# Kernel tuning notes

Hardware: AMD Instinct MI355X
Metric: run time of the kernel (lower is better)

Reference implementation:

```python
import jax, jax.numpy as jnp
import numpy as np

NA, NB = 50000, 10000        # node counts for types 'a' and 'b'
D_IN, D_OUT = 32, 64         # input feature dim, GRU hidden / GAT out dim
EA2A, EA2B, EB2A = 800000, 400000, 400000


def setup_inputs() -> dict:
    key = jax.random.key(0)
    ks = jax.random.split(key, 17)
    f32 = jnp.float32
    inp = {
        'x_a': jax.random.normal(ks[0], (NA, D_IN), f32),
        'x_b': jax.random.normal(ks[1], (NB, D_IN), f32),
        'h_a': jax.random.normal(ks[2], (NA, D_OUT), f32),
        'h_b': jax.random.normal(ks[3], (NB, D_OUT), f32),
        # stacked params: axis0 = gate (z,r,n); axis1 = node type (a,b) or edge type (a2a,a2b,b2a)
        'Wx': jax.random.normal(ks[4], (3, 2, D_IN, D_OUT), f32) * 0.05,
        'bx': jax.random.normal(ks[5], (3, 2, D_OUT), f32) * 0.05,
        'gat_ws': jax.random.normal(ks[6], (3, 3, D_OUT, D_OUT), f32) * 0.05,
        'gat_wd': jax.random.normal(ks[7], (3, 3, D_OUT, D_OUT), f32) * 0.05,
        'gat_as': jax.random.normal(ks[8], (3, 3, D_OUT), f32) * 0.05,
        'gat_ad': jax.random.normal(ks[9], (3, 3, D_OUT), f32) * 0.05,
        'gat_b': jax.random.normal(ks[10], (3, 3, D_OUT), f32) * 0.05,
        'ea2a_src': jax.random.randint(ks[11], (EA2A,), 0, NA, jnp.int32),
        'ea2a_dst': jax.random.randint(ks[12], (EA2A,), 0, NA, jnp.int32),
        'ea2b_src': jax.random.randint(ks[13], (EA2B,), 0, NA, jnp.int32),
        'ea2b_dst': jax.random.randint(ks[14], (EA2B,), 0, NB, jnp.int32),
        'eb2a_src': jax.random.randint(ks[15], (EB2A,), 0, NB, jnp.int32),
        'eb2a_dst': jax.random.randint(ks[16], (EB2A,), 0, NA, jnp.int32),
    }
    return inp


def _gat(hs, hd, src, dst, w_s, w_d, a_s, a_d, b, n_dst):
    """Single-head GATConv (PyG semantics, add_self_loops=False)."""
    xs = hs @ w_s                                   # [Ns, D] transformed sources
    xd = hd @ w_d                                   # [Nd, D] transformed destinations
    al_s = xs @ a_s                                 # [Ns]
    al_d = xd @ a_d                                 # [Nd]
    e = jax.nn.leaky_relu(al_s[src] + al_d[dst], 0.2)   # [E] raw attention logits
    m = jax.ops.segment_max(e, dst, num_segments=n_dst)
    m = jnp.where(jnp.isfinite(m), m, 0.0)          # empty segments -> 0 (unused)
    ex = jnp.exp(e - m[dst])
    denom = jax.ops.segment_sum(ex, dst, num_segments=n_dst)
    alpha = ex / (denom[dst] + 1e-16)               # segment softmax over in-edges
    out = jax.ops.segment_sum(alpha[:, None] * xs[src], dst, num_segments=n_dst)
    return out + b


def _hetero_conv(ha, hb, ws, wd, a_s, a_d, b, edges):
    """HeteroConv with sum aggregation across edge types per destination type."""
    (sa2a, da2a), (sa2b, da2b), (sb2a, db2a) = edges
    out_a = (_gat(ha, ha, sa2a, da2a, ws[0], wd[0], a_s[0], a_d[0], b[0], NA)
             + _gat(hb, ha, sb2a, db2a, ws[2], wd[2], a_s[2], a_d[2], b[2], NA))
    out_b = _gat(ha, hb, sa2b, da2b, ws[1], wd[1], a_s[1], a_d[1], b[1], NB)
    return out_a, out_b


def reference(x_a, x_b, h_a, h_b, Wx, bx, gat_ws, gat_wd, gat_as, gat_ad, gat_b,
              ea2a_src, ea2a_dst, ea2b_src, ea2b_dst, eb2a_src, eb2a_dst):
    edges = ((ea2a_src, ea2a_dst), (ea2b_src, ea2b_dst), (eb2a_src, eb2a_dst))

    def gate(g, ha_in, hb_in, act):
        ca, cb = _hetero_conv(ha_in, hb_in, gat_ws[g], gat_wd[g],
                              gat_as[g], gat_ad[g], gat_b[g], edges)
        ga = act(x_a @ Wx[g, 0] + ca + bx[g, 0])
        gb = act(x_b @ Wx[g, 1] + cb + bx[g, 1])
        return ga, gb

    z_a, z_b = gate(0, h_a, h_b, jax.nn.sigmoid)          # update gate
    r_a, r_b = gate(1, h_a, h_b, jax.nn.sigmoid)          # reset gate
    n_a, n_b = gate(2, r_a * h_a, r_b * h_b, jnp.tanh)    # candidate state
    new_a = (1.0 - z_a) * n_a + z_a * h_a
    new_b = (1.0 - z_b) * n_b + z_b * h_b
    return jnp.concatenate([new_a, new_b], axis=0)        # [NA+NB, D_OUT]
```

## Files before the change

kernel.cpp:

```cpp
#include <hip/hip_runtime.h>
#include <hip/hip_bf16.h>
#include <cstddef>
#include <cstdint>

#define NA 50000
#define NB 10000
#define D_IN 32
#define D_OUT 64
#define EA2A 800000
#define EA2B 400000
#define EB2A 400000
#define NCAT (NA + NB + NA)
#define ETOT (EA2A + EA2B + EB2A)
#define NCHUNK 8
#define CHUNK (NCAT / NCHUNK)
#define NSLICE 64
#define ESLICE (ETOT / NSLICE)

typedef unsigned int u32;
typedef unsigned short u16;
typedef __attribute__((ext_vector_type(8))) short short8_t;
typedef __attribute__((ext_vector_type(4))) float f32x4;
typedef __attribute__((ext_vector_type(2))) float f32x2;

__device__ __forceinline__ u32 bf16r(float x) {
    u32 u = __float_as_uint(x);
    u += 0x7fffu + ((u >> 16) & 1u);
    return u >> 16;
}
__device__ __forceinline__ float ubf(u32 bits) { return __uint_as_float(bits); }
__device__ __forceinline__ float sigm(float x) { return 1.f / (1.f + __expf(-x)); }
__device__ __forceinline__ u32 cvtpk(float lo, float hi) {
    u32 r;
    asm("v_cvt_pk_bf16_f32 %0, %1, %2" : "=v"(r) : "v"(lo), "v"(hi));
    return r;
}
__device__ __forceinline__ void pkfma(f32x2& acc, f32x2 x, f32x2 p) {
    asm("v_pk_fma_f32 %0, %1, %2, %0" : "+v"(acc) : "v"(x), "v"(p));
}

template <int CTRL, int RM>
__device__ __forceinline__ float dppf(float v) {
    return __int_as_float(__builtin_amdgcn_update_dpp(0, __float_as_int(v), CTRL, RM, 0xf, true));
}
__device__ __forceinline__ float wsum64(float v) {
    v += dppf<0x111, 0xf>(v);
    v += dppf<0x112, 0xf>(v);
    v += dppf<0x114, 0xf>(v);
    v += dppf<0x118, 0xf>(v);
    v += dppf<0x142, 0xa>(v);
    v += dppf<0x143, 0xc>(v);
    return __int_as_float(__builtin_amdgcn_readlane(__float_as_int(v), 63));
}

struct MmArgs {
    const float* H; int ntiles;
    const float* W0; const float* W1;
    void* XS;
    const float* SW[8]; const float* SA[8]; float* SOUT[8];
    int sstride; int nsc;
};

template <int NMAT>
__global__ void __launch_bounds__(256) gemm_mfma(MmArgs a)
{
    __shared__ float wvec[8][64];
    __shared__ short8_t bfr[NMAT * 8 + 2][64];
    int t = threadIdx.x;
    for (int idx = t; idx < a.nsc * 64; idx += 256) {
        int c = idx >> 6, k = idx & 63;
        const float* w = a.SW[c] + k * 64;
        const float* av = a.SA[c];
        float s = 0.f;
#pragma unroll 16
        for (int e = 0; e < 64; ++e) s = fmaf(w[e], av[e], s);
        wvec[c][k] = s;
    }
    __syncthreads();
    for (int idx = t; idx < NMAT * 8 * 64; idx += 256) {
        int fid = idx >> 6, l = idx & 63;
        int m = fid >> 3, r3 = fid & 7, tn = r3 >> 1, q = r3 & 1;
        const float* W = (NMAT == 2 && m == 1) ? a.W1 : a.W0;
        int kbase = 32 * q + ((l >> 4) << 3);
        int d = 16 * tn + (l & 15);
        short8_t v;
#pragma unroll
        for (int e = 0; e < 8; ++e) v[e] = (short)bf16r(W[(size_t)(kbase + e) * 64 + d]);
        bfr[fid][l] = v;
    }
    for (int idx = t; idx < 128; idx += 256) {
        int q = idx >> 6, l = idx & 63;
        int c = l & 15;
        int kbase = 32 * q + ((l >> 4) << 3);
        short8_t v;
#pragma unroll
        for (int e = 0; e < 8; ++e) v[e] = (c < a.nsc) ? (short)bf16r(wvec[c][kbase + e]) : (short)0;
        bfr[NMAT * 8 + q][l] = v;
    }
    __syncthreads();
    int lane = t & 63, wid = t >> 6;
    short8_t bw[NMAT][4][2], bs0, bs1;
#pragma unroll
    for (int m = 0; m < NMAT; ++m)
#pragma unroll
        for (int tn = 0; tn < 4; ++tn)
#pragma unroll
            for (int q = 0; q < 2; ++q) bw[m][tn][q] = bfr[m * 8 + tn * 2 + q][lane];
    bs0 = bfr[NMAT * 8][lane];
    bs1 = bfr[NMAT * 8 + 1][lane];

    int rl = lane & 15, kg = lane >> 4;
    f32x4 zero = {0.f, 0.f, 0.f, 0.f};
    for (int tile = blockIdx.x * 4 + wid; tile < a.ntiles; tile += gridDim.x * 4) {
        const float4* hp = (const float4*)(a.H + (size_t)(tile * 16 + rl) * 64) + kg * 2;
        float4 a0 = hp[0], a1 = hp[1];
        float4 b0 = hp[8], b1 = hp[9];
        union { short8_t s; u32 w[4]; } A0, A1;
        A0.w[0] = cvtpk(a0.x, a0.y); A0.w[1] = cvtpk(a0.z, a0.w);
        A0.w[2] = cvtpk(a1.x, a1.y); A0.w[3] = cvtpk(a1.z, a1.w);
        A1.w[0] = cvtpk(b0.x, b0.y); A1.w[1] = cvtpk(b0.z, b0.w);
        A1.w[2] = cvtpk(b1.x, b1.y); A1.w[3] = cvtpk(b1.z, b1.w);

        f32x4 acc[NMAT][4];
#pragma unroll
        for (int m = 0; m < NMAT; ++m)
#pragma unroll
            for (int tn = 0; tn < 4; ++tn) {
                f32x4 c0 = __builtin_amdgcn_mfma_f32_16x16x32_bf16(A0.s, bw[m][tn][0], zero, 0, 0, 0);
                acc[m][tn] = __builtin_amdgcn_mfma_f32_16x16x32_bf16(A1.s, bw[m][tn][1], c0, 0, 0, 0);
            }
        f32x4 accs = __builtin_amdgcn_mfma_f32_16x16x32_bf16(A0.s, bs0, zero, 0, 0, 0);
        accs = __builtin_amdgcn_mfma_f32_16x16x32_bf16(A1.s, bs1, accs, 0, 0, 0);

        int rbase = tile * 16 + kg * 4;
        if (NMAT == 2) {
            u32* xo = (u32*)a.XS;
#pragma unroll
            for (int tn = 0; tn < 4; ++tn) {
                int d = tn * 16 + rl;
#pragma unroll
                for (int j = 0; j < 4; ++j)
                    xo[(size_t)(rbase + j) * 64 + d] = cvtpk(acc[0][tn][j], acc[1][tn][j]);
            }
        } else {
            u16* xo = (u16*)a.XS;
#pragma unroll
            for (int tn = 0; tn < 4; ++tn) {
                int d = tn * 16 + rl;
#pragma unroll
                for (int j = 0; j < 4; ++j)
                    xo[(size_t)(rbase + j) * 64 + d] = (u16)bf16r(acc[0][tn][j]);
            }
        }
        if (rl < a.nsc) {
            float* so = a.SOUT[rl];
#pragma unroll
            for (int j = 0; j < 4; ++j) so[(size_t)(rbase + j) * a.sstride] = accs[j];
        }
    }
}

__global__ void __launch_bounds__(256) gemm_x_k(
    const float* __restrict__ xA, const float* __restrict__ xB,
    const float* __restrict__ Wx, const float* __restrict__ bx, const float* __restrict__ gb,
    u32* __restrict__ dzrA, u32* __restrict__ dzrB,
    u16* __restrict__ dnA, u16* __restrict__ dnB)
{
    __shared__ float Wsh[3 * 2048];
    __shared__ float cb[3 * 64];
    int t = threadIdx.x;
    int blk = blockIdx.x;
    bool isA = blk < (NA / 8);
    int ty = isA ? 0 : 1;
#pragma unroll
    for (int g = 0; g < 3; ++g) {
        const float4* s = (const float4*)(Wx + (size_t)(g * 2 + ty) * 2048);
        float4* d = (float4*)&Wsh[g * 2048];
        for (int i = t; i < 512; i += 256) d[i] = s[i];
    }
    if (t < 192) {
        int g = t >> 6, d = t & 63;
        float c = bx[(g * 2 + ty) * 64 + d];
        if (isA) c += gb[(g * 3 + 0) * 64 + d] + gb[(g * 3 + 2) * 64 + d];
        else     c += gb[(g * 3 + 1) * 64 + d];
        cb[t] = c;
    }
    __syncthreads();
    int lane = t & 63, wid = t >> 6;
    const float* X = isA ? xA : xB;
    int N = isA ? NA : NB;
    int rbase = (isA ? blk : blk - NA / 8) * 8 + wid * 2;
    float cz = cb[lane], cr = cb[64 + lane], cn = cb[128 + lane];
#pragma unroll
    for (int rr = 0; rr < 2; ++rr) {
        int r = rbase + rr;
        if (r >= N) break;
        float xv = (lane < 32) ? X[(size_t)r * 32 + lane] : 0.f;
        float az = cz, ar = cr, an = cn;
#pragma unroll
        for (int k = 0; k < 32; ++k) {
            float xk = __shfl(xv, k, 64);
            az = fmaf(xk, Wsh[k * 64 + lane], az);
            ar = fmaf(xk, Wsh[2048 + k * 64 + lane], ar);
            an = fmaf(xk, Wsh[4096 + k * 64 + lane], an);
        }
        u32 zr = bf16r(az) | (bf16r(ar) << 16);
        u16 nn = (u16)bf16r(an);
        if (isA) { dzrA[(size_t)r * 64 + lane] = zr; dnA[(size_t)r * 64 + lane] = nn; }
        else     { dzrB[(size_t)r * 64 + lane] = zr; dnB[(size_t)r * 64 + lane] = nn; }
    }
}

__global__ void __launch_bounds__(512) hist_k(
    const int* __restrict__ d0, const int* __restrict__ d1, const int* __restrict__ d2,
    u16* __restrict__ partial)
{
    __shared__ int hcnt[CHUNK];
    int k = blockIdx.x & (NCHUNK - 1);
    int s = blockIdx.x / NCHUNK;
    int lo = k * CHUNK;
    for (int i = threadIdx.x; i < CHUNK; i += 512) hcnt[i] = 0;
    __syncthreads();
    int e0 = s * ESLICE, e1 = e0 + ESLICE;
    for (int e = e0 + threadIdx.x; e < e1; e += 512) {
        int g;
        if (e < EA2A) g = d0[e];
        else if (e < EA2A + EA2B) g = NA + d1[e - EA2A];
        else g = NA + NB + d2[e - EA2A - EA2B];
        u32 rel = (u32)(g - lo);
        if (rel < CHUNK) atomicAdd(&hcnt[rel], 1);
    }
    __syncthreads();
    u16* po = partial + (size_t)s * NCAT + lo;
    for (int i = threadIdx.x; i < CHUNK; i += 512) po[i] = (u16)hcnt[i];
}

__global__ void scan_partial(const u16* __restrict__ partial, int* __restrict__ bsum, int N)
{
    __shared__ int sd[256];
    int t = threadIdx.x;
    int i = blockIdx.x * 256 + t;
    int v = 0;
    if (i < N) {
#pragma unroll 16
        for (int s = 0; s < NSLICE; ++s) v += partial[(size_t)s * NCAT + i];
    }
    sd[t] = v;
    __syncthreads();
    for (int off = 128; off; off >>= 1) {
        if (t < off) sd[t] += sd[t + off];
        __syncthreads();
    }
    if (t == 0) bsum[blockIdx.x] = sd[0];
}

__global__ void __launch_bounds__(512) scan_tops(int* bsum, int nb)
{
    __shared__ int sd[512];
    int t = threadIdx.x;
    int v = (t < nb) ? bsum[t] : 0;
    sd[t] = v;
    __syncthreads();
    for (int off = 1; off < 512; off <<= 1) {
        int add = (t >= off) ? sd[t - off] : 0;
        __syncthreads();
        sd[t] += add;
        __syncthreads();
    }
    if (t < nb) bsum[t] = sd[t] - v;
}

__global__ void scan_final(const u16* __restrict__ partial, const int* __restrict__ bsum,
                           int* __restrict__ rowptr, int* __restrict__ cnt,
                           u32* __restrict__ soff, int N)
{
    __shared__ int sd[256];
    int t = threadIdx.x;
    int i = blockIdx.x * 256 + t;
    int v = 0;
    if (i < N) {
#pragma unroll 16
        for (int s = 0; s < NSLICE; ++s) v += partial[(size_t)s * NCAT + i];
    }
    sd[t] = v;
    __syncthreads();
    for (int off = 1; off < 256; off <<= 1) {
        int add = (t >= off) ? sd[t - off] : 0;
        __syncthreads();
        sd[t] += add;
        __syncthreads();
    }
    if (i < N) {
        int rpi = bsum[blockIdx.x] + sd[t] - v;
        rowptr[i] = rpi;
        cnt[i] = v;
        int run = rpi;
#pragma unroll 16
        for (int s = 0; s < NSLICE; ++s) {
            soff[(size_t)s * NCAT + i] = (u32)run;
            run += partial[(size_t)s * NCAT + i];
        }
    }
}

__global__ void __launch_bounds__(512) fill_k(
    const int* __restrict__ s0, const int* __restrict__ d0,
    const int* __restrict__ s1, const int* __restrict__ d1,
    const int* __restrict__ s2, const int* __restrict__ d2,
    const u32* __restrict__ soff, u16* __restrict__ csr)
{
    __shared__ int fpos[CHUNK];
    int k = blockIdx.x & (NCHUNK - 1);
    int s = blockIdx.x / NCHUNK;
    int lo = k * CHUNK;
    const u32* po = soff + (size_t)s * NCAT + lo;
    for (int i = threadIdx.x; i < CHUNK; i += 512) fpos[i] = (int)po[i];
    __syncthreads();
    int e0 = s * ESLICE, e1 = e0 + ESLICE;
    for (int e = e0 + threadIdx.x; e < e1; e += 512) {
        int g, sidx;
        const int* sp;
        if (e < EA2A) { g = d0[e]; sp = s0; sidx = e; }
        else if (e < EA2A + EA2B) { sidx = e - EA2A; g = NA + d1[sidx]; sp = s1; }
        else { sidx = e - EA2A - EA2B; g = NA + NB + d2[sidx]; sp = s2; }
        u32 rel = (u32)(g - lo);
        if (rel < CHUNK) {
            int src = sp[sidx];
            int p = atomicAdd(&fpos[rel], 1);
            csr[p] = (u16)src;
        }
    }
}

__device__ __forceinline__ void zr_pk(f32x2 azr[4], uint4 v, f32x2 p) {
    f32x2 x;
    x[0] = ubf(v.x << 16); x[1] = ubf(v.x & 0xffff0000u); pkfma(azr[0], x, p);
    x[0] = ubf(v.y << 16); x[1] = ubf(v.y & 0xffff0000u); pkfma(azr[1], x, p);
    x[0] = ubf(v.z << 16); x[1] = ubf(v.z & 0xffff0000u); pkfma(azr[2], x, p);
    x[0] = ubf(v.w << 16); x[1] = ubf(v.w & 0xffff0000u); pkfma(azr[3], x, p);
}

__device__ __forceinline__ void gat_zr_et(
    int gnode, int inode, int lane, int sub, int grp,
    const int* __restrict__ rp, const int* __restrict__ cnt, const u16* __restrict__ csr,
    const float2* __restrict__ als, const float2* __restrict__ ald,
    const uint4* __restrict__ xs,
    float oz[4], float orr[4])
{
    int deg = cnt[gnode];
    if (deg <= 0) return;
    int beg = rp[gnode];
    float2 ad = ald[inode];
    f32x2 azr[4];
#pragma unroll
    for (int q = 0; q < 4; ++q) { azr[q][0] = 0.f; azr[q][1] = 0.f; }
    float szl = 0.f, srl = 0.f;
    for (int base = 0; base < deg; base += 64) {
        int j = base + lane;
        int sj = 0; float pz = 0.f, pr = 0.f;
        if (j < deg) {
            sj = csr[beg + j];
            float2 al = als[sj];
            float tz = al.x + ad.x;
            float tr = al.y + ad.y;
            pz = __expf(fmaxf(tz, 0.2f * tz));
            pr = __expf(fmaxf(tr, 0.2f * tr));
        }
        szl += pz; srl += pr;
        u32 pk = (u32)sj | (bf16r(pz) << 16);
        int c = deg - base; if (c > 64) c = 64;
        int b = 0;
        for (; b + 16 <= c; b += 16) {
            u32 k0 = (u32)__shfl((int)pk, b + grp, 64);
            u32 k1 = (u32)__shfl((int)pk, b + 4 + grp, 64);
            u32 k2 = (u32)__shfl((int)pk, b + 8 + grp, 64);
            u32 k3 = (u32)__shfl((int)pk, b + 12 + grp, 64);
            float q0 = __shfl(pr, b + grp, 64);
            float q1 = __shfl(pr, b + 4 + grp, 64);
            float q2 = __shfl(pr, b + 8 + grp, 64);
            float q3 = __shfl(pr, b + 12 + grp, 64);
            uint4 v0 = xs[(size_t)(k0 & 0xffffu) * 16 + sub];
            uint4 v1 = xs[(size_t)(k1 & 0xffffu) * 16 + sub];
            uint4 v2 = xs[(size_t)(k2 & 0xffffu) * 16 + sub];
            uint4 v3 = xs[(size_t)(k3 & 0xffffu) * 16 + sub];
            f32x2 p;
            p[0] = ubf(k0 & 0xffff0000u); p[1] = q0; zr_pk(azr, v0, p);
            p[0] = ubf(k1 & 0xffff0000u); p[1] = q1; zr_pk(azr, v1, p);
            p[0] = ubf(k2 & 0xffff0000u); p[1] = q2; zr_pk(azr, v2, p);
            p[0] = ubf(k3 & 0xffff0000u); p[1] = q3; zr_pk(azr, v3, p);
        }
        for (; b < c; b += 4) {
            u32 k0 = (u32)__shfl((int)pk, b + grp, 64);
            float q0 = __shfl(pr, b + grp, 64);
            uint4 v0 = xs[(size_t)(k0 & 0xffffu) * 16 + sub];
            f32x2 p;
            p[0] = ubf(k0 & 0xffff0000u); p[1] = q0;
            zr_pk(azr, v0, p);
        }
    }
    float sz = wsum64(szl), sr = wsum64(srl);
    float rz = 1.f / (sz + 1e-16f), rr = 1.f / (sr + 1e-16f);
#pragma unroll
    for (int q = 0; q < 4; ++q) {
        oz[q] = fmaf(azr[q][0], rz, oz[q]);
        orr[q] = fmaf(azr[q][1], rr, orr[q]);
    }
}

__device__ __forceinline__ void n_pk(f32x2 ac[2], uint2 v, f32x2 p) {
    f32x2 x;
    x[0] = ubf(v.x << 16); x[1] = ubf(v.x & 0xffff0000u); pkfma(ac[0], x, p);
    x[0] = ubf(v.y << 16); x[1] = ubf(v.y & 0xffff0000u); pkfma(ac[1], x, p);
}

__device__ __forceinline__ void gat_n_et(
    int gnode, int inode, int lane, int sub, int grp,
    const int* __restrict__ rp, const int* __restrict__ cnt, const u16* __restrict__ csr,
    const float* __restrict__ als, const float* __restrict__ ald,
    const uint2* __restrict__ xs,
    float oa[4])
{
    int deg = cnt[gnode];
    if (deg <= 0) return;
    int beg = rp[gnode];
    float ad = ald[inode];
    f32x2 ac[2];
    ac[0][0] = 0.f; ac[0][1] = 0.f; ac[1][0] = 0.f; ac[1][1] = 0.f;
    float ssl = 0.f;
    for (int base = 0; base < deg; base += 64) {
        int j = base + lane;
        int sj = 0; float pv = 0.f;
        if (j < deg) {
            sj = csr[beg + j];
            float tv = als[sj] + ad;
            pv = __expf(fmaxf(tv, 0.2f * tv));
        }
        ssl += pv;
        u32 pk = (u32)sj | (bf16r(pv) << 16);
        int c = deg - base; if (c > 64) c = 64;
        int b = 0;
        for (; b + 16 <= c; b += 16) {
            u32 k0 = (u32)__shfl((int)pk, b + grp, 64);
            u32 k1 = (u32)__shfl((int)pk, b + 4 + grp, 64);
            u32 k2 = (u32)__shfl((int)pk, b + 8 + grp, 64);
            u32 k3 = (u32)__shfl((int)pk, b + 12 + grp, 64);
            uint2 v0 = xs[(size_t)(k0 & 0xffffu) * 16 + sub];
            uint2 v1 = xs[(size_t)(k1 & 0xffffu) * 16 + sub];
            uint2 v2 = xs[(size_t)(k2 & 0xffffu) * 16 + sub];
            uint2 v3 = xs[(size_t)(k3 & 0xffffu) * 16 + sub];
            f32x2 p;
            p[0] = ubf(k0 & 0xffff0000u); p[1] = p[0]; n_pk(ac, v0, p);
            p[0] = ubf(k1 & 0xffff0000u); p[1] = p[0]; n_pk(ac, v1, p);
            p[0] = ubf(k2 & 0xffff0000u); p[1] = p[0]; n_pk(ac, v2, p);
            p[0] = ubf(k3 & 0xffff0000u); p[1] = p[0]; n_pk(ac, v3, p);
        }
        for (; b < c; b += 4) {
            u32 k0 = (u32)__shfl((int)pk, b + grp, 64);
            uint2 v0 = xs[(size_t)(k0 & 0xffffu) * 16 + sub];
            f32x2 p;
            p[0] = ubf(k0 & 0xffff0000u); p[1] = p[0];
            n_pk(ac, v0, p);
        }
    }
    float ss = wsum64(ssl);
    float rs = 1.f / (ss + 1e-16f);
    oa[0] = fmaf(ac[0][0], rs, oa[0]);
    oa[1] = fmaf(ac[0][1], rs, oa[1]);
    oa[2] = fmaf(ac[1][0], rs, oa[2]);
    oa[3] = fmaf(ac[1][1], rs, oa[3]);
}

struct ZrArgs {
    const int *rp, *cnt;
    const u16 *csr;
    const float2 *als0, *ald0, *als1, *ald1, *als2, *ald2;
    const uint4 *xs0, *xs1, *xs2;
    const u32 *dzrA, *dzrB;
    const float *hA, *hB;
    float *zA, *rhA, *zB, *rhB;
};

__global__ void __launch_bounds__(256) aggregate_zr_k(ZrArgs P)
{
    int t = threadIdx.x, lane = t & 63, wid = t >> 6;
    int sub = lane & 15, grp = lane >> 4;
    float oz[4] = {0.f, 0.f, 0.f, 0.f}, orr[4] = {0.f, 0.f, 0.f, 0.f};
    int blk = blockIdx.x;
    const u32* dzr; const float* Hp; float *Zp, *RHp;
    if (blk < NA / 4) {
        int i = blk * 4 + wid;
        gat_zr_et(i, i, lane, sub, grp, P.rp, P.cnt, P.csr, P.als0, P.ald0, P.xs0, oz, orr);
        gat_zr_et(NA + NB + i, i, lane, sub, grp, P.rp, P.cnt, P.csr, P.als2, P.ald2, P.xs2, oz, orr);
        dzr = P.dzrA + (size_t)i * 64; Hp = P.hA + (size_t)i * 64;
        Zp = P.zA + (size_t)i * 64; RHp = P.rhA + (size_t)i * 64;
    } else {
        int i = (blk - NA / 4) * 4 + wid;
        gat_zr_et(NA + i, i, lane, sub, grp, P.rp, P.cnt, P.csr, P.als1, P.ald1, P.xs1, oz, orr);
        dzr = P.dzrB + (size_t)i * 64; Hp = P.hB + (size_t)i * 64;
        Zp = P.zB + (size_t)i * 64; RHp = P.rhB + (size_t)i * 64;
    }
#pragma unroll
    for (int q = 0; q < 4; ++q) {
        oz[q] += __shfl_xor(oz[q], 16, 64); oz[q] += __shfl_xor(oz[q], 32, 64);
        orr[q] += __shfl_xor(orr[q], 16, 64); orr[q] += __shfl_xor(orr[q], 32, 64);
    }
    if (grp == 0) {
        uint4 d = *(const uint4*)(dzr + sub * 4);
        float4 h = *(const float4*)(Hp + sub * 4);
        float z0 = sigm(oz[0] + ubf(d.x << 16)), r0 = sigm(orr[0] + ubf(d.x & 0xffff0000u)) * h.x;
        float z1 = sigm(oz[1] + ubf(d.y << 16)), r1 = sigm(orr[1] + ubf(d.y & 0xffff0000u)) * h.y;
        float z2 = sigm(oz[2] + ubf(d.z << 16)), r2 = sigm(orr[2] + ubf(d.z & 0xffff0000u)) * h.z;
        float z3 = sigm(oz[3] + ubf(d.w << 16)), r3 = sigm(orr[3] + ubf(d.w & 0xffff0000u)) * h.w;
        *(float4*)(Zp + sub * 4) = make_float4(z0, z1, z2, z3);
        *(float4*)(RHp + sub * 4) = make_float4(r0, r1, r2, r3);
    }
}

struct NArgs {
    const int *rp, *cnt;
    const u16 *csr;
    const float *als0, *ald0, *als1, *ald1, *als2, *ald2;
    const uint2 *xs0, *xs1, *xs2;
    const u16 *dnA, *dnB;
    const float *hA, *hB, *zA, *zB;
    float *outA, *outB;
};

__global__ void __launch_bounds__(256) aggregate_n_k(NArgs P)
{
    int t = threadIdx.x, lane = t & 63, wid = t >> 6;
    int sub = lane & 15, grp = lane >> 4;
    float oa[4] = {0.f, 0.f, 0.f, 0.f};
    int blk = blockIdx.x;
    const u16* dn; const float *Hp, *Zp; float* Op;
    if (blk < NA / 4) {
        int i = blk * 4 + wid;
        gat_n_et(i, i, lane, sub, grp, P.rp, P.cnt, P.csr, P.als0, P.ald0, P.xs0, oa);
        gat_n_et(NA + NB + i, i, lane, sub, grp, P.rp, P.cnt, P.csr, P.als2, P.ald2, P.xs2, oa);
        dn = P.dnA + (size_t)i * 64; Hp = P.hA + (size_t)i * 64;
        Zp = P.zA + (size_t)i * 64; Op = P.outA + (size_t)i * 64;
    } else {
        int i = (blk - NA / 4) * 4 + wid;
        gat_n_et(NA + i, i, lane, sub, grp, P.rp, P.cnt, P.csr, P.als1, P.ald1, P.xs1, oa);
        dn = P.dnB + (size_t)i * 64; Hp = P.hB + (size_t)i * 64;
        Zp = P.zB + (size_t)i * 64; Op = P.outB + (size_t)i * 64;
    }
#pragma unroll
    for (int q = 0; q < 4; ++q) {
        oa[q] += __shfl_xor(oa[q], 16, 64); oa[q] += __shfl_xor(oa[q], 32, 64);
    }
    if (grp == 0) {
        uint2 d = *(const uint2*)(dn + sub * 4);
        float4 h = *(const float4*)(Hp + sub * 4);
        float4 zv = *(const float4*)(Zp + sub * 4);
        float pre[4];
        pre[0] = oa[0] + ubf(d.x << 16);
        pre[1] = oa[1] + ubf(d.x & 0xffff0000u);
        pre[2] = oa[2] + ubf(d.y << 16);
        pre[3] = oa[3] + ubf(d.y & 0xffff0000u);
        float o[4];
        float hh[4] = {h.x, h.y, h.z, h.w};
        float zz[4] = {zv.x, zv.y, zv.z, zv.w};
#pragma unroll
        for (int q = 0; q < 4; ++q) {
            float x2 = fminf(fmaxf(pre[q] * 2.f, -30.f), 30.f);
            float ex = __expf(x2);
            float nv = (ex - 1.f) / (ex + 1.f);
            o[q] = (1.f - zz[q]) * nv + zz[q] * hh[q];
        }
        *(float4*)(Op + sub * 4) = make_float4(o[0], o[1], o[2], o[3]);
    }
}

extern "C" void kernel_launch(void* const* d_in, const int* in_sizes, int n_in,
                              void* d_out, int out_size, void* d_ws, size_t ws_size,
                              hipStream_t stream)
{
    (void)in_sizes; (void)n_in; (void)out_size; (void)ws_size;
    const float* x_a = (const float*)d_in[0];
    const float* x_b = (const float*)d_in[1];
    const float* h_a = (const float*)d_in[2];
    const float* h_b = (const float*)d_in[3];
    const float* Wx  = (const float*)d_in[4];
    const float* bx  = (const float*)d_in[5];
    const float* gws = (const float*)d_in[6];
    const float* gwd = (const float*)d_in[7];
    const float* gas = (const float*)d_in[8];
    const float* gad = (const float*)d_in[9];
    const float* gb  = (const float*)d_in[10];
    const int* ea2a_s = (const int*)d_in[11];
    const int* ea2a_d = (const int*)d_in[12];
    const int* ea2b_s = (const int*)d_in[13];
    const int* ea2b_d = (const int*)d_in[14];
    const int* eb2a_s = (const int*)d_in[15];
    const int* eb2a_d = (const int*)d_in[16];
    float* out = (float*)d_out;

    char* w = (char*)d_ws;
    auto alloc = [&](size_t bytes) -> char* {
        char* p = w;
        w += (bytes + 255) & ~(size_t)255;
        return p;
    };
    char* xsblk = alloc((size_t)(NA + NA + NB) * 64 * 4);
    u32* xs_zr0 = (u32*)xsblk;
    u32* xs_zr1 = (u32*)(xsblk + (size_t)NA * 64 * 4);
    u32* xs_zr2 = (u32*)(xsblk + (size_t)(NA + NA) * 64 * 4);
    u16* xs_n0 = (u16*)xsblk;
    u16* xs_n1 = (u16*)(xsblk + (size_t)NA * 64 * 2);
    u16* xs_n2 = (u16*)(xsblk + (size_t)(NA + NA) * 64 * 2);
    char* alblk = alloc((size_t)(4 * NA + 2 * NB) * 2 * 4);
    float* als_zr0 = (float*)alblk;
    float* als_zr1 = als_zr0 + (size_t)NA * 2;
    float* als_zr2 = als_zr1 + (size_t)NA * 2;
    float* ald_zr0 = als_zr2 + (size_t)NB * 2;
    float* ald_zr1 = ald_zr0 + (size_t)NA * 2;
    float* ald_zr2 = ald_zr1 + (size_t)NB * 2;
    float* als_n0 = (float*)alblk;
    float* als_n1 = als_n0 + NA;
    float* als_n2 = als_n1 + NA;
    float* ald_n0 = als_n2 + NB;
    float* ald_n1 = ald_n0 + NA;
    float* ald_n2 = ald_n1 + NB;
    float* zbuf  = (float*)alloc((size_t)(NA + NB) * 64 * 4);
    float* rhbuf = (float*)alloc((size_t)(NA + NB) * 64 * 4);
    u32* dzrA = (u32*)alloc((size_t)NA * 64 * 4);
    u32* dzrB = (u32*)alloc((size_t)NB * 64 * 4);
    u16* dnA = (u16*)alloc((size_t)NA * 64 * 2);
    u16* dnB = (u16*)alloc((size_t)NB * 64 * 2);
    u16* partial = (u16*)alloc((size_t)NSLICE * NCAT * 2);
    u32* soff    = (u32*)alloc((size_t)NSLICE * NCAT * 4);
    int* cnt = (int*)alloc((size_t)NCAT * 4);
    int* rp  = (int*)alloc((size_t)NCAT * 4);
    u16* csr = (u16*)alloc((size_t)ETOT * 2);
    int* bsum = (int*)alloc(512 * 4);

    const int nbC = (NCAT + 255) / 256;

    hist_k<<<NCHUNK * NSLICE, 512, 0, stream>>>(ea2a_d, ea2b_d, eb2a_d, partial);
    scan_partial<<<nbC, 256, 0, stream>>>(partial, bsum, NCAT);
    scan_tops<<<1, 512, 0, stream>>>(bsum, nbC);
    scan_final<<<nbC, 256, 0, stream>>>(partial, bsum, rp, cnt, soff, NCAT);
    fill_k<<<NCHUNK * NSLICE, 512, 0, stream>>>(ea2a_s, ea2a_d, ea2b_s, ea2b_d, eb2a_s, eb2a_d,
                                                soff, csr);

    gemm_x_k<<<(NA + NB) / 8, 256, 0, stream>>>(x_a, x_b, Wx, bx, gb, dzrA, dzrB, dnA, dnB);

    float* rh_a = rhbuf;
    float* rh_b = rhbuf + (size_t)NA * 64;
    float* z_a = zbuf;
    float* z_b = zbuf + (size_t)NA * 64;

    {
        MmArgs a{};
        a.H = h_a; a.ntiles = NA / 16;
        a.W0 = gws + 0 * 4096; a.W1 = gws + 3 * 4096;
        a.XS = xs_zr0;
        a.SW[0] = gws + 0 * 4096; a.SA[0] = gas + 0 * 64; a.SOUT[0] = als_zr0;
        a.SW[1] = gws + 3 * 4096; a.SA[1] = gas + 3 * 64; a.SOUT[1] = als_zr0 + 1;
        a.SW[2] = gws + 1 * 4096; a.SA[2] = gas + 1 * 64; a.SOUT[2] = als_zr1;
        a.SW[3] = gws + 4 * 4096; a.SA[3] = gas + 4 * 64; a.SOUT[3] = als_zr1 + 1;
        a.SW[4] = gwd + 0 * 4096; a.SA[4] = gad + 0 * 64; a.SOUT[4] = ald_zr0;
        a.SW[5] = gwd + 3 * 4096; a.SA[5] = gad + 3 * 64; a.SOUT[5] = ald_zr0 + 1;
        a.SW[6] = gwd + 2 * 4096; a.SA[6] = gad + 2 * 64; a.SOUT[6] = ald_zr2;
        a.SW[7] = gwd + 5 * 4096; a.SA[7] = gad + 5 * 64; a.SOUT[7] = ald_zr2 + 1;
        a.sstride = 2; a.nsc = 8;
        gemm_mfma<2><<<320, 256, 0, stream>>>(a);
    }
    {
        MmArgs a{};
        a.H = h_a; a.ntiles = NA / 16;
        a.W0 = gws + 1 * 4096; a.W1 = gws + 4 * 4096;
        a.XS = xs_zr1;
        a.sstride = 1; a.nsc = 0;
        gemm_mfma<2><<<320, 256, 0, stream>>>(a);
    }
    {
        MmArgs a{};
        a.H = h_b; a.ntiles = NB / 16;
        a.W0 = gws + 2 * 4096; a.W1 = gws + 5 * 4096;
        a.XS = xs_zr2;
        a.SW[0] = gws + 2 * 4096; a.SA[0] = gas + 2 * 64; a.SOUT[0] = als_zr2;
        a.SW[1] = gws + 5 * 4096; a.SA[1] = gas + 5 * 64; a.SOUT[1] = als_zr2 + 1;
        a.SW[2] = gwd + 1 * 4096; a.SA[2] = gad + 1 * 64; a.SOUT[2] = ald_zr1;
        a.SW[3] = gwd + 4 * 4096; a.SA[3] = gad + 4 * 64; a.SOUT[3] = ald_zr1 + 1;
        a.sstride = 2; a.nsc = 4;
        gemm_mfma<2><<<80, 256, 0, stream>>>(a);
    }

    {
        ZrArgs P{};
        P.rp = rp; P.cnt = cnt; P.csr = csr;
        P.als0 = (const float2*)als_zr0; P.ald0 = (const float2*)ald_zr0;
        P.als1 = (const float2*)als_zr1; P.ald1 = (const float2*)ald_zr1;
        P.als2 = (const float2*)als_zr2; P.ald2 = (const float2*)ald_zr2;
        P.xs0 = (const uint4*)xs_zr0; P.xs1 = (const uint4*)xs_zr1; P.xs2 = (const uint4*)xs_zr2;
        P.dzrA = dzrA; P.dzrB = dzrB;
        P.hA = h_a; P.hB = h_b;
        P.zA = z_a; P.rhA = rh_a; P.zB = z_b; P.rhB = rh_b;
        aggregate_zr_k<<<(NA + NB) / 4, 256, 0, stream>>>(P);
    }

    {
        MmArgs a{};
        a.H = rh_a; a.ntiles = NA / 16;
        a.W0 = gws + 6 * 4096; a.W1 = nullptr;
        a.XS = xs_n0;
        a.SW[0] = gws + 6 * 4096; a.SA[0] = gas + 6 * 64; a.SOUT[0] = als_n0;
        a.SW[1] = gws + 7 * 4096; a.SA[1] = gas + 7 * 64; a.SOUT[1] = als_n1;
        a.SW[2] = gwd + 6 * 4096; a.SA[2] = gad + 6 * 64; a.SOUT[2] = ald_n0;
        a.SW[3] = gwd + 8 * 4096; a.SA[3] = gad + 8 * 64; a.SOUT[3] = ald_n2;
        a.sstride = 1; a.nsc = 4;
        gemm_mfma<1><<<320, 256, 0, stream>>>(a);
    }
    {
        MmArgs a{};
        a.H = rh_a; a.ntiles = NA / 16;
        a.W0 = gws + 7 * 4096; a.W1 = nullptr;
        a.XS = xs_n1;
        a.sstride = 1; a.nsc = 0;
        gemm_mfma<1><<<320, 256, 0, stream>>>(a);
    }
    {
        MmArgs a{};
        a.H = rh_b; a.ntiles = NB / 16;
        a.W0 = gws + 8 * 4096; a.W1 = nullptr;
        a.XS = xs_n2;
        a.SW[0] = gws + 8 * 4096; a.SA[0] = gas + 8 * 64; a.SOUT[0] = als_n2;
        a.SW[1] = gwd + 7 * 4096; a.SA[1] = gad + 7 * 64; a.SOUT[1] = ald_n1;
        a.sstride = 1; a.nsc = 2;
        gemm_mfma<1><<<80, 256, 0, stream>>>(a);
    }

    {
        NArgs P{};
        P.rp = rp; P.cnt = cnt; P.csr = csr;
        P.als0 = als_n0; P.ald0 = ald_n0;
        P.als1 = als_n1; P.ald1 = ald_n1;
        P.als2 = als_n2; P.ald2 = ald_n2;
        P.xs0 = (const uint2*)xs_n0; P.xs1 = (const uint2*)xs_n1; P.xs2 = (const uint2*)xs_n2;
        P.dnA = dnA; P.dnB = dnB;
        P.hA = h_a; P.hB = h_b; P.zA = z_a; P.zB = z_b;
        P.outA = out; P.outB = out + (size_t)NA * 64;
        aggregate_n_k<<<(NA + NB) / 4, 256, 0, stream>>>(P);
    }
}
```

Measured before the change: 316.5 us.

## Widen n-gate gather loads, merge n-gate GEMMs, shrink slice offsets to 16-bit

Three separate changes. The n-gate aggregation now gathers 16-byte rows with 8 lanes per edge instead of 8-byte loads with 16 lanes, so each wave handles 8 edges per step instead of 4, at the cost of more shuffle-reduction stages. The two rh_a GEMMs for the n gate are merged into one two-matrix launch that writes unpacked outputs, so rh_a is read once. The per-slice CSR offsets are stored as 16-bit values relative to the row pointer, which halves that array's traffic; fill_k adds the row pointer back in, and this assumes each node's count within a slice fits in 16 bits.

```diff
diff --git a/kernel.cpp b/kernel.cpp
--- a/kernel.cpp
+++ b/kernel.cpp
@@ -56,12 +56,12 @@
 struct MmArgs {
     const float* H; int ntiles;
     const float* W0; const float* W1;
-    void* XS;
+    void* XS; void* XS1;
     const float* SW[8]; const float* SA[8]; float* SOUT[8];
     int sstride; int nsc;
 };
 
-template <int NMAT>
+template <int NMAT, int PACKED>
 __global__ void __launch_bounds__(256) gemm_mfma(MmArgs a)
 {
     __shared__ float wvec[8][64];
@@ -133,7 +133,7 @@
         accs = __builtin_amdgcn_mfma_f32_16x16x32_bf16(A1.s, bs1, accs, 0, 0, 0);
 
         int rbase = tile * 16 + kg * 4;
-        if (NMAT == 2) {
+        if (NMAT == 2 && PACKED == 1) {
             u32* xo = (u32*)a.XS;
 #pragma unroll
             for (int tn = 0; tn < 4; ++tn) {
@@ -141,6 +141,18 @@
 #pragma unroll
                 for (int j = 0; j < 4; ++j)
                     xo[(size_t)(rbase + j) * 64 + d] = cvtpk(acc[0][tn][j], acc[1][tn][j]);
+            }
+        } else if (NMAT == 2 && PACKED == 0) {
+            u16* xo0 = (u16*)a.XS;
+            u16* xo1 = (u16*)a.XS1;
+#pragma unroll
+            for (int tn = 0; tn < 4; ++tn) {
+                int d = tn * 16 + rl;
+#pragma unroll
+                for (int j = 0; j < 4; ++j) {
+                    xo0[(size_t)(rbase + j) * 64 + d] = (u16)bf16r(acc[0][tn][j]);
+                    xo1[(size_t)(rbase + j) * 64 + d] = (u16)bf16r(acc[1][tn][j]);
+                }
             }
         } else {
             u16* xo = (u16*)a.XS;
@@ -272,7 +284,7 @@
 
 __global__ void scan_final(const u16* __restrict__ partial, const int* __restrict__ bsum,
                            int* __restrict__ rowptr, int* __restrict__ cnt,
-                           u32* __restrict__ soff, int N)
+                           u16* __restrict__ soff, int N)
 {
     __shared__ int sd[256];
     int t = threadIdx.x;
@@ -294,10 +306,10 @@
         int rpi = bsum[blockIdx.x] + sd[t] - v;
         rowptr[i] = rpi;
         cnt[i] = v;
-        int run = rpi;
+        int run = 0;
 #pragma unroll 16
         for (int s = 0; s < NSLICE; ++s) {
-            soff[(size_t)s * NCAT + i] = (u32)run;
+            soff[(size_t)s * NCAT + i] = (u16)run;
             run += partial[(size_t)s * NCAT + i];
         }
     }
@@ -307,14 +319,15 @@
     const int* __restrict__ s0, const int* __restrict__ d0,
     const int* __restrict__ s1, const int* __restrict__ d1,
     const int* __restrict__ s2, const int* __restrict__ d2,
-    const u32* __restrict__ soff, u16* __restrict__ csr)
+    const int* __restrict__ rp, const u16* __restrict__ soff, u16* __restrict__ csr)
 {
     __shared__ int fpos[CHUNK];
     int k = blockIdx.x & (NCHUNK - 1);
     int s = blockIdx.x / NCHUNK;
     int lo = k * CHUNK;
-    const u32* po = soff + (size_t)s * NCAT + lo;
-    for (int i = threadIdx.x; i < CHUNK; i += 512) fpos[i] = (int)po[i];
+    const u16* po = soff + (size_t)s * NCAT + lo;
+    const int* rpo = rp + lo;
+    for (int i = threadIdx.x; i < CHUNK; i += 512) fpos[i] = rpo[i] + (int)po[i];
     __syncthreads();
     int e0 = s * ESLICE, e1 = e0 + ESLICE;
     for (int e = e0 + threadIdx.x; e < e1; e += 512) {
@@ -407,25 +420,28 @@
     }
 }
 
-__device__ __forceinline__ void n_pk(f32x2 ac[2], uint2 v, f32x2 p) {
+__device__ __forceinline__ void n_pk4(f32x2 ac[4], uint4 v, f32x2 p) {
     f32x2 x;
     x[0] = ubf(v.x << 16); x[1] = ubf(v.x & 0xffff0000u); pkfma(ac[0], x, p);
     x[0] = ubf(v.y << 16); x[1] = ubf(v.y & 0xffff0000u); pkfma(ac[1], x, p);
+    x[0] = ubf(v.z << 16); x[1] = ubf(v.z & 0xffff0000u); pkfma(ac[2], x, p);
+    x[0] = ubf(v.w << 16); x[1] = ubf(v.w & 0xffff0000u); pkfma(ac[3], x, p);
 }
 
 __device__ __forceinline__ void gat_n_et(
-    int gnode, int inode, int lane, int sub, int grp,
+    int gnode, int inode, int lane, int sub8, int grp8,
     const int* __restrict__ rp, const int* __restrict__ cnt, const u16* __restrict__ csr,
     const float* __restrict__ als, const float* __restrict__ ald,
-    const uint2* __restrict__ xs,
-    float oa[4])
+    const uint4* __restrict__ xs,
+    f32x2 oa[4])
 {
     int deg = cnt[gnode];
     if (deg <= 0) return;
     int beg = rp[gnode];
     float ad = ald[inode];
-    f32x2 ac[2];
-    ac[0][0] = 0.f; ac[0][1] = 0.f; ac[1][0] = 0.f; ac[1][1] = 0.f;
+    f32x2 ac[4];
+#pragma unroll
+    for (int q = 0; q < 4; ++q) { ac[q][0] = 0.f; ac[q][1] = 0.f; }
     float ssl = 0.f;
     for (int base = 0; base < deg; base += 64) {
         int j = base + lane;
@@ -439,35 +455,33 @@
         u32 pk = (u32)sj | (bf16r(pv) << 16);
         int c = deg - base; if (c > 64) c = 64;
         int b = 0;
-        for (; b + 16 <= c; b += 16) {
-            u32 k0 = (u32)__shfl((int)pk, b + grp, 64);
-            u32 k1 = (u32)__shfl((int)pk, b + 4 + grp, 64);
-            u32 k2 = (u32)__shfl((int)pk, b + 8 + grp, 64);
-            u32 k3 = (u32)__shfl((int)pk, b + 12 + grp, 64);
-            uint2 v0 = xs[(size_t)(k0 & 0xffffu) * 16 + sub];
-            uint2 v1 = xs[(size_t)(k1 & 0xffffu) * 16 + sub];
-            uint2 v2 = xs[(size_t)(k2 & 0xffffu) * 16 + sub];
-            uint2 v3 = xs[(size_t)(k3 & 0xffffu) * 16 + sub];
-            f32x2 p;
-            p[0] = ubf(k0 & 0xffff0000u); p[1] = p[0]; n_pk(ac, v0, p);
-            p[0] = ubf(k1 & 0xffff0000u); p[1] = p[0]; n_pk(ac, v1, p);
-            p[0] = ubf(k2 & 0xffff0000u); p[1] = p[0]; n_pk(ac, v2, p);
-            p[0] = ubf(k3 & 0xffff0000u); p[1] = p[0]; n_pk(ac, v3, p);
-        }
-        for (; b < c; b += 4) {
-            u32 k0 = (u32)__shfl((int)pk, b + grp, 64);
-            uint2 v0 = xs[(size_t)(k0 & 0xffffu) * 16 + sub];
-            f32x2 p;
-            p[0] = ubf(k0 & 0xffff0000u); p[1] = p[0];
-            n_pk(ac, v0, p);
+        for (; b + 32 <= c; b += 32) {
+            u32 kk[4];
+#pragma unroll
+            for (int u = 0; u < 4; ++u) kk[u] = (u32)__shfl((int)pk, b + 8 * u + grp8, 64);
+            uint4 vv[4];
+#pragma unroll
+            for (int u = 0; u < 4; ++u) vv[u] = xs[(size_t)(kk[u] & 0xffffu) * 8 + sub8];
+#pragma unroll
+            for (int u = 0; u < 4; ++u) {
+                f32x2 p; p[0] = ubf(kk[u] & 0xffff0000u); p[1] = p[0];
+                n_pk4(ac, vv[u], p);
+            }
+        }
+        for (; b < c; b += 8) {
+            u32 k0 = (u32)__shfl((int)pk, b + grp8, 64);
+            uint4 v0 = xs[(size_t)(k0 & 0xffffu) * 8 + sub8];
+            f32x2 p; p[0] = ubf(k0 & 0xffff0000u); p[1] = p[0];
+            n_pk4(ac, v0, p);
         }
     }
     float ss = wsum64(ssl);
     float rs = 1.f / (ss + 1e-16f);
-    oa[0] = fmaf(ac[0][0], rs, oa[0]);
-    oa[1] = fmaf(ac[0][1], rs, oa[1]);
-    oa[2] = fmaf(ac[1][0], rs, oa[2]);
-    oa[3] = fmaf(ac[1][1], rs, oa[3]);
+#pragma unroll
+    for (int q = 0; q < 4; ++q) {
+        oa[q][0] = fmaf(ac[q][0], rs, oa[q][0]);
+        oa[q][1] = fmaf(ac[q][1], rs, oa[q][1]);
+    }
 }
 
 struct ZrArgs {
@@ -520,7 +534,7 @@
     const int *rp, *cnt;
     const u16 *csr;
     const float *als0, *ald0, *als1, *ald1, *als2, *ald2;
-    const uint2 *xs0, *xs1, *xs2;
+    const uint4 *xs0, *xs1, *xs2;
     const u16 *dnA, *dnB;
     const float *hA, *hB, *zA, *zB;
     float *outA, *outB;
@@ -529,46 +543,56 @@
 __global__ void __launch_bounds__(256) aggregate_n_k(NArgs P)
 {
     int t = threadIdx.x, lane = t & 63, wid = t >> 6;
-    int sub = lane & 15, grp = lane >> 4;
-    float oa[4] = {0.f, 0.f, 0.f, 0.f};
+    int sub8 = lane & 7, grp8 = lane >> 3;
+    f32x2 oa[4];
+#pragma unroll
+    for (int q = 0; q < 4; ++q) { oa[q][0] = 0.f; oa[q][1] = 0.f; }
     int blk = blockIdx.x;
     const u16* dn; const float *Hp, *Zp; float* Op;
     if (blk < NA / 4) {
         int i = blk * 4 + wid;
-        gat_n_et(i, i, lane, sub, grp, P.rp, P.cnt, P.csr, P.als0, P.ald0, P.xs0, oa);
-        gat_n_et(NA + NB + i, i, lane, sub, grp, P.rp, P.cnt, P.csr, P.als2, P.ald2, P.xs2, oa);
+        gat_n_et(i, i, lane, sub8, grp8, P.rp, P.cnt, P.csr, P.als0, P.ald0, P.xs0, oa);
+        gat_n_et(NA + NB + i, i, lane, sub8, grp8, P.rp, P.cnt, P.csr, P.als2, P.ald2, P.xs2, oa);
         dn = P.dnA + (size_t)i * 64; Hp = P.hA + (size_t)i * 64;
         Zp = P.zA + (size_t)i * 64; Op = P.outA + (size_t)i * 64;
     } else {
         int i = (blk - NA / 4) * 4 + wid;
-        gat_n_et(NA + i, i, lane, sub, grp, P.rp, P.cnt, P.csr, P.als1, P.ald1, P.xs1, oa);
+        gat_n_et(NA + i, i, lane, sub8, grp8, P.rp, P.cnt, P.csr, P.als1, P.ald1, P.xs1, oa);
         dn = P.dnB + (size_t)i * 64; Hp = P.hB + (size_t)i * 64;
         Zp = P.zB + (size_t)i * 64; Op = P.outB + (size_t)i * 64;
     }
 #pragma unroll
     for (int q = 0; q < 4; ++q) {
-        oa[q] += __shfl_xor(oa[q], 16, 64); oa[q] += __shfl_xor(oa[q], 32, 64);
-    }
-    if (grp == 0) {
-        uint2 d = *(const uint2*)(dn + sub * 4);
-        float4 h = *(const float4*)(Hp + sub * 4);
-        float4 zv = *(const float4*)(Zp + sub * 4);
-        float pre[4];
-        pre[0] = oa[0] + ubf(d.x << 16);
-        pre[1] = oa[1] + ubf(d.x & 0xffff0000u);
-        pre[2] = oa[2] + ubf(d.y << 16);
-        pre[3] = oa[3] + ubf(d.y & 0xffff0000u);
-        float o[4];
-        float hh[4] = {h.x, h.y, h.z, h.w};
-        float zz[4] = {zv.x, zv.y, zv.z, zv.w};
-#pragma unroll
-        for (int q = 0; q < 4; ++q) {
+#pragma unroll
+        for (int e = 0; e < 2; ++e) {
+            oa[q][e] += __shfl_xor(oa[q][e], 8, 64);
+            oa[q][e] += __shfl_xor(oa[q][e], 16, 64);
+            oa[q][e] += __shfl_xor(oa[q][e], 32, 64);
+        }
+    }
+    if (grp8 == 0) {
+        uint4 d = *(const uint4*)(dn + sub8 * 8);
+        float4 h0 = *(const float4*)(Hp + sub8 * 8);
+        float4 h1 = *(const float4*)(Hp + sub8 * 8 + 4);
+        float4 zv0 = *(const float4*)(Zp + sub8 * 8);
+        float4 zv1 = *(const float4*)(Zp + sub8 * 8 + 4);
+        float pre[8];
+        pre[0] = oa[0][0] + ubf(d.x << 16); pre[1] = oa[0][1] + ubf(d.x & 0xffff0000u);
+        pre[2] = oa[1][0] + ubf(d.y << 16); pre[3] = oa[1][1] + ubf(d.y & 0xffff0000u);
+        pre[4] = oa[2][0] + ubf(d.z << 16); pre[5] = oa[2][1] + ubf(d.z & 0xffff0000u);
+        pre[6] = oa[3][0] + ubf(d.w << 16); pre[7] = oa[3][1] + ubf(d.w & 0xffff0000u);
+        float hh[8] = {h0.x, h0.y, h0.z, h0.w, h1.x, h1.y, h1.z, h1.w};
+        float zz[8] = {zv0.x, zv0.y, zv0.z, zv0.w, zv1.x, zv1.y, zv1.z, zv1.w};
+        float o[8];
+#pragma unroll
+        for (int q = 0; q < 8; ++q) {
             float x2 = fminf(fmaxf(pre[q] * 2.f, -30.f), 30.f);
             float ex = __expf(x2);
             float nv = (ex - 1.f) / (ex + 1.f);
             o[q] = (1.f - zz[q]) * nv + zz[q] * hh[q];
         }
-        *(float4*)(Op + sub * 4) = make_float4(o[0], o[1], o[2], o[3]);
+        *(float4*)(Op + sub8 * 8) = make_float4(o[0], o[1], o[2], o[3]);
+        *(float4*)(Op + sub8 * 8 + 4) = make_float4(o[4], o[5], o[6], o[7]);
     }
 }
 
@@ -629,7 +653,7 @@
     u16* dnA = (u16*)alloc((size_t)NA * 64 * 2);
     u16* dnB = (u16*)alloc((size_t)NB * 64 * 2);
     u16* partial = (u16*)alloc((size_t)NSLICE * NCAT * 2);
-    u32* soff    = (u32*)alloc((size_t)NSLICE * NCAT * 4);
+    u16* soff    = (u16*)alloc((size_t)NSLICE * NCAT * 2);
     int* cnt = (int*)alloc((size_t)NCAT * 4);
     int* rp  = (int*)alloc((size_t)NCAT * 4);
     u16* csr = (u16*)alloc((size_t)ETOT * 2);
@@ -642,7 +666,7 @@
     scan_tops<<<1, 512, 0, stream>>>(bsum, nbC);
     scan_final<<<nbC, 256, 0, stream>>>(partial, bsum, rp, cnt, soff, NCAT);
     fill_k<<<NCHUNK * NSLICE, 512, 0, stream>>>(ea2a_s, ea2a_d, ea2b_s, ea2b_d, eb2a_s, eb2a_d,
-                                                soff, csr);
+                                                rp, soff, csr);
 
     gemm_x_k<<<(NA + NB) / 8, 256, 0, stream>>>(x_a, x_b, Wx, bx, gb, dzrA, dzrB, dnA, dnB);
 
@@ -665,7 +689,7 @@
         a.SW[6] = gwd + 2 * 4096; a.SA[6] = gad + 2 * 64; a.SOUT[6] = ald_zr2;
         a.SW[7] = gwd + 5 * 4096; a.SA[7] = gad + 5 * 64; a.SOUT[7] = ald_zr2 + 1;
         a.sstride = 2; a.nsc = 8;
-        gemm_mfma<2><<<320, 256, 0, stream>>>(a);
+        gemm_mfma<2, 1><<<320, 256, 0, stream>>>(a);
     }
     {
         MmArgs a{};
@@ -673,7 +697,7 @@
         a.W0 = gws + 1 * 4096; a.W1 = gws + 4 * 4096;
         a.XS = xs_zr1;
         a.sstride = 1; a.nsc = 0;
-        gemm_mfma<2><<<320, 256, 0, stream>>>(a);
+        gemm_mfma<2, 1><<<320, 256, 0, stream>>>(a);
     }
     {
         MmArgs a{};
@@ -685,7 +709,7 @@
         a.SW[2] = gwd + 1 * 4096; a.SA[2] = gad + 1 * 64; a.SOUT[2] = ald_zr1;
         a.SW[3] = gwd + 4 * 4096; a.SA[3] = gad + 4 * 64; a.SOUT[3] = ald_zr1 + 1;
         a.sstride = 2; a.nsc = 4;
-        gemm_mfma<2><<<80, 256, 0, stream>>>(a);
+        gemm_mfma<2, 1><<<80, 256, 0, stream>>>(a);
     }
 
     {
@@ -704,22 +728,14 @@
     {
         MmArgs a{};
         a.H = rh_a; a.ntiles = NA / 16;
-        a.W0 = gws + 6 * 4096; a.W1 = nullptr;
-        a.XS = xs_n0;
+        a.W0 = gws + 6 * 4096; a.W1 = gws + 7 * 4096;
+        a.XS = xs_n0; a.XS1 = xs_n1;
         a.SW[0] = gws + 6 * 4096; a.SA[0] = gas + 6 * 64; a.SOUT[0] = als_n0;
         a.SW[1] = gws + 7 * 4096; a.SA[1] = gas + 7 * 64; a.SOUT[1] = als_n1;
         a.SW[2] = gwd + 6 * 4096; a.SA[2] = gad + 6 * 64; a.SOUT[2] = ald_n0;
         a.SW[3] = gwd + 8 * 4096; a.SA[3] = gad + 8 * 64; a.SOUT[3] = ald_n2;
         a.sstride = 1; a.nsc = 4;
-        gemm_mfma<1><<<320, 256, 0, stream>>>(a);
-    }
-    {
-        MmArgs a{};
-        a.H = rh_a; a.ntiles = NA / 16;
-        a.W0 = gws + 7 * 4096; a.W1 = nullptr;
-        a.XS = xs_n1;
-        a.sstride = 1; a.nsc = 0;
-        gemm_mfma<1><<<320, 256, 0, stream>>>(a);
+        gemm_mfma<2, 0><<<320, 256, 0, stream>>>(a);
     }
     {
         MmArgs a{};
@@ -729,7 +745,7 @@
         a.SW[0] = gws + 8 * 4096; a.SA[0] = gas + 8 * 64; a.SOUT[0] = als_n2;
         a.SW[1] = gwd + 7 * 4096; a.SA[1] = gad + 7 * 64; a.SOUT[1] = ald_n1;
         a.sstride = 1; a.nsc = 2;
-        gemm_mfma<1><<<80, 256, 0, stream>>>(a);
+        gemm_mfma<1, 1><<<80, 256, 0, stream>>>(a);
     }
 
     {
@@ -738,7 +754,7 @@
         P.als0 = als_n0; P.ald0 = ald_n0;
         P.als1 = als_n1; P.ald1 = ald_n1;
         P.als2 = als_n2; P.ald2 = ald_n2;
-        P.xs0 = (const uint2*)xs_n0; P.xs1 = (const uint2*)xs_n1; P.xs2 = (const uint2*)xs_n2;
+        P.xs0 = (const uint4*)xs_n0; P.xs1 = (const uint4*)xs_n1; P.xs2 = (const uint4*)xs_n2;
         P.dnA = dnA; P.dnB = dnB;
         P.hA = h_a; P.hB = h_b; P.zA = z_a; P.zB = z_b;
         P.outA = out; P.outB = out + (size_t)NA * 64;
```

After: 316.5 us. Within noise of the previous version (-0.0%).
